# Kernel tuning notes

Hardware: AMD Instinct MI355X
Metric: run time of the kernel (lower is better)

## Reference

```python
import jax, jax.numpy as jnp
import numpy as np

H = 2048          # hidden_size
HK = 16           # linear_num_key_heads
HV = 32           # linear_num_value_heads
DK = 128          # linear_key_head_dim
DV = 128          # linear_value_head_dim
KW = 4            # linear_conv_kernel_dim
KEY_DIM = HK * DK   # 2048
VAL_DIM = HV * DV   # 4096
CONV_DIM = 2 * KEY_DIM + VAL_DIM  # 8192
T = 4096
EPS = 1e-6


def setup_inputs() -> dict:
    key = jax.random.key(0)
    ks = jax.random.split(key, 8)
    w = lambda k, shape, sc=0.02: (jax.random.normal(k, shape, jnp.float32) * sc)
    return {
        "hidden_states": jax.random.normal(ks[0], (T, H), jnp.float32),
        "W_qkvz": w(ks[1], (H, 2 * KEY_DIM + 2 * VAL_DIM)),   # q,k,v,z merged proj
        "W_ba": w(ks[2], (H, 2 * HV)),                        # b,a merged proj
        "conv_w": w(ks[3], (CONV_DIM, KW), 0.1),              # depthwise causal conv
        "A_log": jnp.log(jax.random.uniform(ks[4], (HV,), jnp.float32, 1.0, 16.0)),
        "dt_bias": jnp.ones((HV,), jnp.float32),
        "norm_w": jnp.ones((DV,), jnp.float32),
        "W_out": w(ks[5], (VAL_DIM, H)),
    }


def _l2norm(x):
    return x * jax.lax.rsqrt(jnp.sum(x * x, axis=-1, keepdims=True) + 1e-6)


def reference(hidden_states, W_qkvz, W_ba, conv_w, A_log, dt_bias, norm_w, W_out):
    T_ = hidden_states.shape[0]
    # 1. merged input projections
    qkvz = hidden_states @ W_qkvz                     # [T, 2*key+2*val]
    ba = hidden_states @ W_ba                         # [T, 2*HV]
    q, k, v, z = jnp.split(qkvz, [KEY_DIM, 2 * KEY_DIM, 2 * KEY_DIM + VAL_DIM], axis=-1)
    b, a = jnp.split(ba, 2, axis=-1)

    # 2. short causal depthwise conv1d over q|k|v (z is NOT convolved), then SiLU
    qkv = jnp.concatenate([q, k, v], axis=-1)         # [T, CONV_DIM]
    xp = jnp.pad(qkv, ((KW - 1, 0), (0, 0)))
    y = sum(xp[j:j + T_] * conv_w[:, j] for j in range(KW))
    qkv = jax.nn.silu(y)
    q, k, v = jnp.split(qkv, [KEY_DIM, 2 * KEY_DIM], axis=-1)

    q = _l2norm(q.reshape(T_, HK, DK)) * (DK ** -0.5)
    k = _l2norm(k.reshape(T_, HK, DK))
    v = v.reshape(T_, HV, DV)
    z = z.reshape(T_, HV, DV)

    # GQA-style head expansion
    r = HV // HK
    q = jnp.repeat(q, r, axis=1)                      # [T, HV, DK]
    k = jnp.repeat(k, r, axis=1)

    # gating / delta coefficients
    g = -jnp.exp(A_log) * jax.nn.softplus(a + dt_bias)  # [T, HV] log-decay
    beta = jax.nn.sigmoid(b)                            # [T, HV]

    # 3. gated delta rule recurrence: S_t = exp(g_t)*S + beta_t*k_t(v_t - k_t^T exp(g_t) S)
    def step(S, inp):
        q_t, k_t, v_t, g_t, b_t = inp
        S = S * jnp.exp(g_t)[:, None, None]             # [HV, DK, DV]
        kv = jnp.einsum('hd,hdv->hv', k_t, S)
        delta = (v_t - kv) * b_t[:, None]
        S = S + jnp.einsum('hd,hv->hdv', k_t, delta)
        o_t = jnp.einsum('hd,hdv->hv', q_t, S)
        return S, o_t

    S0 = jnp.zeros((HV, DK, DV), jnp.float32)
    _, o = jax.lax.scan(step, S0, (q, k, v, g, beta))   # o: [T, HV, DV]

    # 4. gated RMSNorm (norm_before_gate=True): rmsnorm(o)*w, then * silu(z)
    var = jnp.mean(o * o, axis=-1, keepdims=True)
    o = o * jax.lax.rsqrt(var + EPS) * norm_w
    o = o * jax.nn.silu(z)

    # 5. output projection
    return o.reshape(T_, VAL_DIM) @ W_out
```

## Files before the change

### kernel.cpp

```cpp
#include <hip/hip_runtime.h>
#include <hip/hip_bf16.h>

#define T_LEN 4096
#define H_DIM 2048
#define HKn 16
#define HVn 32
#define DKn 128
#define DVn 128
#define KEY_DIM 2048
#define VAL_DIM 4096

typedef unsigned int u32;
typedef unsigned short u16;
typedef __attribute__((ext_vector_type(8))) short bf16x8;
typedef __attribute__((ext_vector_type(4))) float f32x4;

__device__ __forceinline__ u16 f2bf(float x){
  u32 u = __float_as_uint(x);
  u32 r = (u + 0x7fffu + ((u>>16)&1u)) >> 16;
  return (u16)r;
}
__device__ __forceinline__ float bf2f(u32 b){ return __uint_as_float(b<<16); }
__device__ __forceinline__ u32 packbf(float a, float b){ return (u32)f2bf(a) | ((u32)f2bf(b)<<16); }

__global__ __launch_bounds__(256) void k_cvt(const float* __restrict__ in, u16* __restrict__ out, int n){
  int i = (blockIdx.x*256 + threadIdx.x)*8;
  if (i >= n) return;
  float4 a = *(const float4*)(in+i);
  float4 b = *(const float4*)(in+i+4);
  uint4 o;
  o.x = packbf(a.x,a.y); o.y = packbf(a.z,a.w);
  o.z = packbf(b.x,b.y); o.w = packbf(b.z,b.w);
  *(uint4*)(out+i) = o;
}

__global__ __launch_bounds__(256) void k_tcvt(const float* __restrict__ in, u16* __restrict__ out, int R, int C){
  __shared__ float tile[32][33];
  int c0 = blockIdx.x*32, r0 = blockIdx.y*32;
  int tx = threadIdx.x & 31, ty = threadIdx.x >> 5;
#pragma unroll
  for (int i=0;i<4;++i) tile[ty+8*i][tx] = in[(size_t)(r0+ty+8*i)*C + c0+tx];
  __syncthreads();
#pragma unroll
  for (int i=0;i<4;++i) out[(size_t)(c0+ty+8*i)*R + r0+tx] = f2bf(tile[tx][ty+8*i]);
}

__global__ __launch_bounds__(256) void k_ba(const float* __restrict__ X, const float* __restrict__ W,
    const float* __restrict__ A_log, const float* __restrict__ dt_bias,
    float* __restrict__ gT, float* __restrict__ bT){
  int tid = threadIdx.x;
  int t = blockIdx.x*4 + (tid>>6);
  int j = tid & 63;
  const float* xr = X + (size_t)t*H_DIM;
  float acc = 0.f;
  for (int k=0;k<H_DIM;k+=4){
    float4 xv = *(const float4*)(xr+k);
    acc += xv.x*W[(size_t)(k+0)*64 + j];
    acc += xv.y*W[(size_t)(k+1)*64 + j];
    acc += xv.z*W[(size_t)(k+2)*64 + j];
    acc += xv.w*W[(size_t)(k+3)*64 + j];
  }
  if (j < HVn) {
    bT[(size_t)j*T_LEN + t] = 1.f/(1.f+__expf(-acc));
  } else {
    int h = j - HVn;
    float x = acc + dt_bias[h];
    float sp = (x > 20.f) ? x : log1pf(__expf(x));
    gT[(size_t)h*T_LEN + t] = -__expf(A_log[h]) * sp;
  }
}

typedef const __attribute__((address_space(1))) u32* gas_t;
typedef __attribute__((address_space(3))) u32* las_t;
__device__ __forceinline__ void gld16(const void* g, void* l){
  __builtin_amdgcn_global_load_lds((gas_t)g, (las_t)l, 16, 0, 0);
}
__device__ __forceinline__ f32x4 mf(bf16x8 a, bf16x8 b, f32x4 c){
  return __builtin_amdgcn_mfma_f32_16x16x32_bf16(a,b,c,0,0,0);
}

#define G2_LDS 131072
#define SWX(a) ((a) ^ ((((a)>>9)&1)<<5))

template<int WRITE_BF16>
__global__ __launch_bounds__(512) void k_g256(const u16* __restrict__ A, const u16* __restrict__ BT,
    void* __restrict__ C1, void* __restrict__ C2, int NS, int M, int N, int K){
  extern __shared__ char sm[];
  const int tid=threadIdx.x, lane=tid&63, wave=tid>>6;
  const int fr=lane&15, fq=lane>>4;
  const int wm=wave>>2, wn=wave&3;
  const int nbm = M>>8, nwg = nbm*(N>>8);
  const int cpx = nwg>>3;
  const int swz = ((int)blockIdx.x & 7)*cpx + ((int)blockIdx.x >> 3);
  const int m0 = (swz % nbm) << 8, n0 = (swz / nbm) << 8;
  const int NK = K >> 5;

  f32x4 acc[8][4];
#pragma unroll
  for (int i=0;i<8;++i)
#pragma unroll
    for (int j=0;j<4;++j) acc[i][j] = (f32x4){0.f,0.f,0.f,0.f};

  auto stageA=[&](int kt){
    char* base = sm + (size_t)(kt&3)*32768;
#pragma unroll
    for (int ld=0; ld<2; ++ld){
      int p = ld*8192 + wave*1024 + lane*16;
      int a = SWX(p);
      gld16((const char*)A + ((size_t)(m0 + (a>>6))*K + kt*32)*2 + (a&63), base + p);
    }
  };
  auto stageB=[&](int kt){
    char* base = sm + (size_t)(kt&3)*32768 + 16384;
#pragma unroll
    for (int ld=0; ld<2; ++ld){
      int p = ld*8192 + wave*1024 + lane*16;
      int a = SWX(p);
      gld16((const char*)BT + ((size_t)(n0 + (a>>6))*K + kt*32)*2 + (a&63), base + p);
    }
  };

  stageA(0); stageB(0); stageA(1); stageB(1); stageA(2); stageB(2);
  __syncthreads();

  for (int kt=0; kt<NK; ++kt){
    const char* bufA = sm + (size_t)(kt&3)*32768;
    const char* bufB = bufA + 16384;
    bf16x8 bfr[4], afr[4];
#pragma unroll
    for (int j=0;j<4;++j){
      int a = (wn*64 + j*16 + fr)*64 + fq*16;
      bfr[j] = *(const bf16x8*)(bufB + SWX(a));
    }
#pragma unroll
    for (int i=0;i<4;++i){
      int a = (wm*128 + i*16 + fr)*64 + fq*16;
      afr[i] = *(const bf16x8*)(bufA + SWX(a));
    }
    if (kt+3 < NK) stageA(kt+3);
    asm volatile("s_barrier" ::: "memory");
    __builtin_amdgcn_s_setprio(1);
#pragma unroll
    for (int i=0;i<4;++i)
#pragma unroll
      for (int j=0;j<4;++j) acc[i][j] = mf(afr[i], bfr[j], acc[i][j]);
    __builtin_amdgcn_s_setprio(0);
    asm volatile("s_barrier" ::: "memory");
#pragma unroll
    for (int i=0;i<4;++i){
      int a = (wm*128 + 64 + i*16 + fr)*64 + fq*16;
      afr[i] = *(const bf16x8*)(bufA + SWX(a));
    }
    if (kt+3 < NK) stageB(kt+3);
    asm volatile("s_barrier" ::: "memory");
    __builtin_amdgcn_s_setprio(1);
#pragma unroll
    for (int i=0;i<4;++i)
#pragma unroll
      for (int j=0;j<4;++j) acc[4+i][j] = mf(afr[i], bfr[j], acc[4+i][j]);
    __builtin_amdgcn_s_setprio(0);
    asm volatile("s_waitcnt vmcnt(8)" ::: "memory");
    asm volatile("s_barrier" ::: "memory");
  }

#pragma unroll
  for (int mt=0; mt<8; ++mt)
#pragma unroll
    for (int nt=0; nt<4; ++nt){
      int row = m0 + wm*128 + mt*16 + fq*4;
      int col = n0 + wn*64 + nt*16 + fr;
#pragma unroll
      for (int r=0;r<4;++r){
        float v = acc[mt][nt][r];
        if (col < NS){
          if (WRITE_BF16) ((u16*)C1)[(size_t)(row+r)*NS + col] = f2bf(v);
          else            ((float*)C1)[(size_t)(row+r)*NS + col] = v;
        } else {
          if (WRITE_BF16) ((u16*)C2)[(size_t)(row+r)*(N-NS) + col-NS] = f2bf(v);
          else            ((float*)C2)[(size_t)(row+r)*(N-NS) + col-NS] = v;
        }
      }
    }
}

template<int WRITE_BF16>
__global__ __launch_bounds__(256) void k_gemm(const u16* __restrict__ A, const u16* __restrict__ BT,
                                              void* __restrict__ C1, void* __restrict__ C2, int NS,
                                              int M, int N, int K){
  __shared__ __align__(16) u16 As[128*32];
  __shared__ __align__(16) u16 Bs[128*32];
  int tid = threadIdx.x, lane = tid & 63, wave = tid >> 6;
  int wr = wave >> 1, wc = wave & 1;
  int m0 = blockIdx.x*128, n0 = blockIdx.y*128;
  int fr = lane & 15, fq = lane >> 4;
  f32x4 zero = {0.f,0.f,0.f,0.f};
  f32x4 acc[4][4];
#pragma unroll
  for (int m=0;m<4;++m)
#pragma unroll
    for (int n=0;n<4;++n) acc[m][n] = zero;

  for (int kt=0; kt<K; kt+=32){
#pragma unroll
    for (int it=0; it<2; ++it){
      int c = (it*4 + wave)*64 + lane;
      int row = c >> 2, kc = (c & 3) << 3;
      gld16(A  + (size_t)(m0+row)*K + kt + kc, (char*)As + (size_t)(it*4+wave)*1024);
      gld16(BT + (size_t)(n0+row)*K + kt + kc, (char*)Bs + (size_t)(it*4+wave)*1024);
    }
    __syncthreads();
    bf16x8 af[4], bff[4];
#pragma unroll
    for (int m=0;m<4;++m) af[m]  = *(const bf16x8*)(As + (wr*64 + m*16 + fr)*32 + fq*8);
#pragma unroll
    for (int n=0;n<4;++n) bff[n] = *(const bf16x8*)(Bs + (wc*64 + n*16 + fr)*32 + fq*8);
#pragma unroll
    for (int m=0;m<4;++m)
#pragma unroll
      for (int n=0;n<4;++n)
        acc[m][n] = mf(af[m], bff[n], acc[m][n]);
    __syncthreads();
  }
#pragma unroll
  for (int m=0;m<4;++m)
#pragma unroll
    for (int n=0;n<4;++n){
      int row = m0 + wr*64 + m*16 + fq*4;
      int col = n0 + wc*64 + n*16 + fr;
#pragma unroll
      for (int r=0;r<4;++r){
        float v = acc[m][n][r];
        if (col < NS){
          if (WRITE_BF16) ((u16*)C1)[(size_t)(row+r)*NS + col] = f2bf(v);
          else            ((float*)C1)[(size_t)(row+r)*NS + col] = v;
        } else {
          if (WRITE_BF16) ((u16*)C2)[(size_t)(row+r)*(N-NS) + col-NS] = f2bf(v);
          else            ((float*)C2)[(size_t)(row+r)*(N-NS) + col-NS] = v;
        }
      }
    }
}

__global__ __launch_bounds__(256) void k_conv(const u16* __restrict__ qkv, const float* __restrict__ cw,
    u16* __restrict__ qn, u16* __restrict__ kn, u16* __restrict__ vv){
  int t = blockIdx.x;
  int region = blockIdx.y;
  int c = region*2048 + threadIdx.x*8;
  float wgt[8][4];
#pragma unroll
  for (int i=0;i<8;++i){
    float4 wv = *(const float4*)(cw + (size_t)(c+i)*4);
    wgt[i][0]=wv.x; wgt[i][1]=wv.y; wgt[i][2]=wv.z; wgt[i][3]=wv.w;
  }
  float y[8];
#pragma unroll
  for (int i=0;i<8;++i) y[i]=0.f;
#pragma unroll
  for (int j=0;j<4;++j){
    int tt = t + j - 3;
    if (tt < 0) continue;
    uint4 raw = *(const uint4*)(qkv + (size_t)tt*8192 + c);
    float xv[8];
    xv[0]=bf2f(raw.x&0xffffu); xv[1]=bf2f(raw.x>>16);
    xv[2]=bf2f(raw.y&0xffffu); xv[3]=bf2f(raw.y>>16);
    xv[4]=bf2f(raw.z&0xffffu); xv[5]=bf2f(raw.z>>16);
    xv[6]=bf2f(raw.w&0xffffu); xv[7]=bf2f(raw.w>>16);
#pragma unroll
    for (int i=0;i<8;++i) y[i] += xv[i]*wgt[i][j];
  }
#pragma unroll
  for (int i=0;i<8;++i){ y[i] = y[i] / (1.f + __expf(-y[i])); }

  if (region <= 1){
    float ss = 0.f;
#pragma unroll
    for (int i=0;i<8;++i) ss += y[i]*y[i];
    ss += __shfl_xor(ss,1); ss += __shfl_xor(ss,2);
    ss += __shfl_xor(ss,4); ss += __shfl_xor(ss,8);
    float sc = 1.f/sqrtf(ss + 1e-6f);
    if (region==0) sc *= 0.08838834764831845f;
#pragma unroll
    for (int i=0;i<8;++i) y[i]*=sc;
    u16* dst = (region==0 ? qn : kn) + (size_t)t*KEY_DIM + (c - region*2048);
    *(uint4*)dst = make_uint4(packbf(y[0],y[1]),packbf(y[2],y[3]),packbf(y[4],y[5]),packbf(y[6],y[7]));
  } else {
    u16* dst = vv + (size_t)t*VAL_DIM + (c - 4096);
    *(uint4*)dst = make_uint4(packbf(y[0],y[1]),packbf(y[2],y[3]),packbf(y[4],y[5]),packbf(y[6],y[7]));
  }
}

#define P1_K    0
#define P1_Q    16384
#define P1_KT   32768
#define P1_NBP  49152
#define P1_AQ   57344
#define P1_DT   65536
#define P1_WMT  73728
#define P1_NBD  81920
#define P1_TII  86016
#define P1_R1T  90112
#define P1_TAB  94208
#define P1_SIZE 95296

#define SW7(r,cb) ((cb) ^ (((r)&7)<<4))
#define SW3(r,cb) ((cb) ^ (((r)&3)<<4))
#define aK(r,cb)   (P1_K   + (r)*256 + SW7(r,cb))
#define aQ2(r,cb)  (P1_Q   + (r)*256 + SW7(r,cb))
#define aKT(d,cb)  (P1_KT  + (d)*128 + SW7(d,cb))
#define aNBP(t,cb) (P1_NBP + (t)*128 + SW7(t,cb))
#define aAQ(t,cb)  (P1_AQ  + (t)*128 + SW7(t,cb))
#define aDT(s,cb)  (P1_DT  + (s)*128 + SW7(s,cb))
#define aWMT(s,cb) (P1_WMT + (s)*128 + SW7(s,cb))
#define aTII(b,r,cb) (P1_TII + (b)*1024 + (r)*64 + SW3(r,cb))
#define aR1T(v,cb)   (P1_R1T + (v)*64 + SW3(v,cb))

__global__ __launch_bounds__(256) void k_prep(const u16* __restrict__ qn, const u16* __restrict__ kn,
    const float* __restrict__ gT, const float* __restrict__ bT,
    u16* __restrict__ aqmg, u16* __restrict__ kwmg, float* __restrict__ tabg){
  extern __shared__ char sm[];
  const int tid=threadIdx.x, lane=tid&63, wave=tid>>6;
  const int fr=lane&15, fq=lane>>4;
  const int b=blockIdx.x, h=b>>6, c=b&63, kh=h>>1;
  const f32x4 z4={0.f,0.f,0.f,0.f};
  for (int off=P1_DT+tid*16; off<P1_TAB; off+=4096) *(uint4*)(sm+off)=make_uint4(0,0,0,0);
  {
    int srow = wave*4 + (lane>>4);
    int pb = (lane&15)*16;
#pragma unroll
    for (int r=0;r<4;++r){
      int row=r*16+srow;
      int gcb = pb ^ ((row&7)<<4);
      gld16((const char*)kn + ((size_t)((c<<6)+row)*KEY_DIM + kh*DKn)*2 + gcb, sm + P1_K + r*4096 + wave*1024);
      gld16((const char*)qn + ((size_t)((c<<6)+row)*KEY_DIM + kh*DKn)*2 + gcb, sm + P1_Q + r*4096 + wave*1024);
    }
  }
  float* TB=(float*)(sm+P1_TAB);
  if (wave==0){
    int t=lane;
    float gv=gT[(size_t)h*T_LEN+(c<<6)+t];
    float bv=bT[(size_t)h*T_LEN+(c<<6)+t];
    float s=gv;
    for(int o2=1;o2<64;o2<<=1){ float u=__shfl_up(s,o2,64); if(lane>=o2) s+=u; }
    float cgL=__shfl(s,63,64);
    float gam=__expf(s);
    TB[t]=s; TB[64+t]=gam; TB[128+t]=__expf(cgL-s); TB[192+t]=bv;
    float* tg=tabg+(size_t)b*192;
    tg[t]=gam; tg[64+t]=bv;
    if(t==0) tg[128]=__expf(cgL);
  }
  __syncthreads();
#pragma unroll
  for (int dd=0;dd<2;++dd){
    int tp=tid&31, d0=((tid>>5)+dd*8)*8;
    bf16x8 r0=*(const bf16x8*)(sm+aK(2*tp,d0*2));
    bf16x8 r1=*(const bf16x8*)(sm+aK(2*tp+1,d0*2));
#pragma unroll
    for(int j=0;j<8;++j){
      u32 pk=((u32)(u16)r0[j])|((u32)(u16)r1[j]<<16);
      *(u32*)(sm+aKT(d0+j,tp*4))=pk;
    }
  }
  const int ra=(wave>>1)*32, rb=(wave&1)*32;
  f32x4 kq[2][2], qk[2][2];
#pragma unroll
  for(int ta=0;ta<2;++ta)
#pragma unroll
  for(int tb=0;tb<2;++tb){ kq[ta][tb]=z4; qk[ta][tb]=z4; }
#pragma unroll
  for(int kk=0;kk<4;++kk){
    int cb=kk*64+fq*16;
    bf16x8 Ak0=*(const bf16x8*)(sm+aK(ra+fr,cb));
    bf16x8 Ak1=*(const bf16x8*)(sm+aK(ra+16+fr,cb));
    bf16x8 Aq0=*(const bf16x8*)(sm+aQ2(ra+fr,cb));
    bf16x8 Aq1=*(const bf16x8*)(sm+aQ2(ra+16+fr,cb));
    bf16x8 Bk0=*(const bf16x8*)(sm+aK(rb+fr,cb));
    bf16x8 Bk1=*(const bf16x8*)(sm+aK(rb+16+fr,cb));
    if(ra>=rb)      { kq[0][0]=mf(Ak0,Bk0,kq[0][0]); qk[0][0]=mf(Aq0,Bk0,qk[0][0]); }
    if(ra>=rb+16)   { kq[0][1]=mf(Ak0,Bk1,kq[0][1]); qk[0][1]=mf(Aq0,Bk1,qk[0][1]); }
    if(ra+16>=rb)   { kq[1][0]=mf(Ak1,Bk0,kq[1][0]); qk[1][0]=mf(Aq1,Bk0,qk[1][0]); }
    if(ra+16>=rb+16){ kq[1][1]=mf(Ak1,Bk1,kq[1][1]); qk[1][1]=mf(Aq1,Bk1,qk[1][1]); }
  }
  {
    const float* cg=TB; const float* Be=TB+192;
#pragma unroll
    for(int ta=0;ta<2;++ta)
#pragma unroll
    for(int tb=0;tb<2;++tb){
      int tab=ra+16*ta, tbb=rb+16*tb;
#pragma unroll
      for(int p=0;p<4;++p){
        int t=tab+fq*4+p, s2=tbb+fr;
        float e=__expf(cg[t]-cg[s2]);
        float nv=(s2<t)? -Be[t]*kq[ta][tb][p]*e : 0.f;
        *(u16*)(sm+aNBP(t,s2*2)) = (tbb<tab)? f2bf(nv):(u16)0;
        if(tbb==tab) ((float*)(sm+P1_NBD))[(tab>>4)*256+(fq*4+p)*16+fr]=nv;
        float av=(s2<=t)? qk[ta][tb][p]*e : 0.f;
        *(u16*)(sm+aAQ(t,s2*2)) = f2bf(av);
      }
    }
  }
  __syncthreads();
  {
    int r=lane&15;
    const float* nb=(const float*)(sm+P1_NBD)+wave*256+r*16;
    float n[16], t_[16];
#pragma unroll
    for(int j=0;j<16;++j){ n[j]=nb[j]; t_[j]=(j==r)?1.f:0.f; }
#pragma unroll
    for(int s=0;s<15;++s){
      float tsj[16];
#pragma unroll
      for(int j=0;j<16;++j)
        tsj[j]=__int_as_float(__builtin_amdgcn_ds_bpermute(s*4,__float_as_int(t_[j])));
      if(r>s){
#pragma unroll
        for(int j=0;j<16;++j) t_[j]=fmaf(n[s],tsj[j],t_[j]);
      }
    }
    if(lane<16){
      u32 pk[8];
#pragma unroll
      for(int j=0;j<8;++j) pk[j]=packbf(t_[2*j],t_[2*j+1]);
      *(uint4*)(sm+aTII(wave,r,0)) =make_uint4(pk[0],pk[1],pk[2],pk[3]);
      *(uint4*)(sm+aTII(wave,r,16))=make_uint4(pk[4],pk[5],pk[6],pk[7]);
    }
  }
  __syncthreads();
  {
    const float* WV=TB+128;
    int vb=16*wave;
    for(int i=0;i<4;++i){
      f32x4 acc;
#pragma unroll
      for(int p=0;p<4;++p) acc[p]=(vb+fr==16*i+fq*4+p)?1.f:0.f;
      int np=(i+1)>>1;
      for(int jp=0;jp<np;++jp){
        bf16x8 A=*(const bf16x8*)(sm+aNBP(16*i+fr,jp*64+fq*16));
        bf16x8 B=*(const bf16x8*)(sm+aDT(vb+fr,jp*64+fq*16));
        acc=mf(A,B,acc);
      }
      uint2 w1; w1.x=packbf(acc[0],acc[1]); w1.y=packbf(acc[2],acc[3]);
      *(uint2*)(sm+aR1T(vb+fr,fq*8))=w1;
      bf16x8 At=*(const bf16x8*)(sm+aTII(i,fr,fq*16));
      bf16x8 Bt=*(const bf16x8*)(sm+aR1T(vb+fr,fq*16));
      f32x4 dl=mf(At,Bt,z4);
      int s0=16*i+fq*4;
      uint2 wd; wd.x=packbf(dl[0],dl[1]); wd.y=packbf(dl[2],dl[3]);
      *(uint2*)(sm+aDT(vb+fr,s0*2))=wd;
      uint2 ww; ww.x=packbf(dl[0]*WV[s0],dl[1]*WV[s0+1]); ww.y=packbf(dl[2]*WV[s0+2],dl[3]*WV[s0+3]);
      *(uint2*)(sm+aWMT(vb+fr,s0*2))=ww;
    }
  }
  __syncthreads();
  {
    u16* aout = aqmg + (size_t)b*4096;
#pragma unroll
    for(int ts=0;ts<4;++ts){
      f32x4 acc=z4;
#pragma unroll
      for(int jp=0;jp<2;++jp){
        bf16x8 A=*(const bf16x8*)(sm+aAQ(16*wave+fr,jp*64+fq*16));
        bf16x8 B=*(const bf16x8*)(sm+aDT(16*ts+fr,jp*64+fq*16));
        acc=mf(A,B,acc);
      }
#pragma unroll
      for(int p=0;p<4;++p){
        int t=16*wave+fq*4+p, s=16*ts+fr;
        aout[(t*128 + ((s*2)^((t&7)<<4)))>>1]=f2bf(acc[p]);
      }
    }
    u16* kout = kwmg + (size_t)b*8192;
#pragma unroll
    for(int j=0;j<2;++j){
      int dt=wave+4*j;
#pragma unroll
      for(int st=0;st<4;++st){
        f32x4 acc=z4;
#pragma unroll
        for(int jp=0;jp<2;++jp){
          bf16x8 A=*(const bf16x8*)(sm+aKT(16*dt+fr,jp*64+fq*16));
          bf16x8 B=*(const bf16x8*)(sm+aWMT(16*st+fr,jp*64+fq*16));
          acc=mf(A,B,acc);
        }
#pragma unroll
        for(int p=0;p<4;++p){
          int d=16*dt+fq*4+p, s=16*st+fr;
          kout[(d*128 + ((s*2)^((d&7)<<4)))>>1]=f2bf(acc[p]);
        }
      }
    }
  }
}

#define P2_K(b)   ((b)*16384)
#define P2_Q(b)   (32768 + (b)*16384)
#define P2_W(b)   (65536 + (b)*16384)
#define P2_M(b)   (98304 + (b)*8192)
#define P2_TAB(b) (114688 + (b)*1024)
#define P2_ST(b)  (116736 + (b)*4096)
#define P2_R0T    124928
#define P2_SIZE   126976

#define bKx(b,r,cb)  (P2_K(b) + (r)*256 + SW7(r,cb))
#define bQx(b,r,cb)  (P2_Q(b) + (r)*256 + SW7(r,cb))
#define bWx(b,d,cb)  (P2_W(b) + (d)*128 + SW7(d,cb))
#define bMx(b,t,cb)  (P2_M(b) + (t)*128 + SW7(t,cb))
#define bSTx(b,v,cb) (P2_ST(b) + (v)*256 + SW7(v,cb))
#define bRx(v,cb)    (P2_R0T + (v)*128 + SW7(v,cb))

__global__ __launch_bounds__(256) void k_state(const u16* __restrict__ qn, const u16* __restrict__ kn,
    const u16* __restrict__ vv, const u16* __restrict__ aqmg, const u16* __restrict__ kwmg,
    const float* __restrict__ tabg, float* __restrict__ o){
  extern __shared__ char sm[];
  const int tid=threadIdx.x, lane=tid&63, wave=tid>>6;
  const int fr=lane&15, fq=lane>>4;
  const int h=blockIdx.x&31, vs=(blockIdx.x>>5)*16, kh=h>>1;
  const f32x4 z4={0.f,0.f,0.f,0.f};
  for(int off=116736+tid*16; off<124928; off+=4096) *(uint4*)(sm+off)=make_uint4(0,0,0,0);

  auto stage=[&](int c,int b){
    int srow=wave*4+(lane>>4);
    int pb2=(lane&15)*16;
#pragma unroll
    for(int r=0;r<4;++r){
      int row=r*16+srow;
      int gcb=pb2^((row&7)<<4);
      gld16((const char*)kn + ((size_t)((c<<6)+row)*KEY_DIM + kh*DKn)*2 + gcb, sm + P2_K(b)+r*4096+wave*1024);
      gld16((const char*)qn + ((size_t)((c<<6)+row)*KEY_DIM + kh*DKn)*2 + gcb, sm + P2_Q(b)+r*4096+wave*1024);
    }
    const char* wsrc=(const char*)kwmg + (size_t)(h*64+c)*16384;
#pragma unroll
    for(int r=0;r<4;++r)
      gld16(wsrc + r*4096 + wave*1024 + lane*16, sm + P2_W(b)+r*4096+wave*1024);
    const char* msrc=(const char*)aqmg + (size_t)(h*64+c)*8192;
#pragma unroll
    for(int r=0;r<2;++r)
      gld16(msrc + r*4096 + wave*1024 + lane*16, sm + P2_M(b)+r*4096+wave*1024);
    if(wave==0)
      gld16((const char*)tabg + (size_t)(h*64+c)*768 + lane*16, sm + P2_TAB(b));
  };
  u16 vl[4];
  auto loadV=[&](int c){
#pragma unroll
    for(int p=0;p<4;++p)
      vl[p]=vv[(size_t)((c<<6)+16*wave+fq*4+p)*VAL_DIM + h*DVn + vs + fr];
  };

  f32x4 S0=z4, S1=z4;
  stage(0,0); loadV(0);
  __syncthreads();

  for(int c=0;c<64;++c){
    int b=c&1;
    const float* TBf=(const float*)(sm+P2_TAB(b));
    f32x4 ks=z4;
#pragma unroll
    for(int kk=0;kk<4;++kk)
      ks=mf(*(const bf16x8*)(sm+bKx(b,16*wave+fr,kk*64+fq*16)),
            *(const bf16x8*)(sm+bSTx(b,fr,kk*64+fq*16)), ks);
    float r0v[4];
#pragma unroll
    for(int p=0;p<4;++p){
      int t=16*wave+fq*4+p;
      r0v[p]=TBf[64+t]*(bf2f(vl[p]) - TBf[t]*ks[p]);
    }
    uint2 rw; rw.x=packbf(r0v[0],r0v[1]); rw.y=packbf(r0v[2],r0v[3]);
    *(uint2*)(sm+bRx(fr,32*wave+8*fq))=rw;
    __syncthreads();
    if(c<63) stage(c+1,b^1);
    f32x4 qs=z4;
#pragma unroll
    for(int kk=0;kk<4;++kk)
      qs=mf(*(const bf16x8*)(sm+bQx(b,16*wave+fr,kk*64+fq*16)),
            *(const bf16x8*)(sm+bSTx(b,fr,kk*64+fq*16)), qs);
#pragma unroll
    for(int p=0;p<4;++p) qs[p]*=TBf[16*wave+fq*4+p];
#pragma unroll
    for(int jp=0;jp<2;++jp)
      qs=mf(*(const bf16x8*)(sm+bMx(b,16*wave+fr,jp*64+fq*16)),
            *(const bf16x8*)(sm+bRx(fr,jp*64+fq*16)), qs);
#pragma unroll
    for(int p=0;p<4;++p)
      o[(size_t)((c<<6)+16*wave+fq*4+p)*VAL_DIM + h*DVn + vs + fr]=qs[p];
    if(c<63) loadV(c+1);
    float gl=TBf[128];
    S0[0]*=gl;S0[1]*=gl;S0[2]*=gl;S0[3]*=gl;
    S1[0]*=gl;S1[1]*=gl;S1[2]*=gl;S1[3]*=gl;
#pragma unroll
    for(int jp=0;jp<2;++jp){
      bf16x8 Br=*(const bf16x8*)(sm+bRx(fr,jp*64+fq*16));
      S0=mf(*(const bf16x8*)(sm+bWx(b,16*wave+fr,jp*64+fq*16)), Br, S0);
      S1=mf(*(const bf16x8*)(sm+bWx(b,16*(wave+4)+fr,jp*64+fq*16)), Br, S1);
    }
    uint2 s0w; s0w.x=packbf(S0[0],S0[1]); s0w.y=packbf(S0[2],S0[3]);
    *(uint2*)(sm+bSTx(b^1,fr,32*wave+8*fq))=s0w;
    uint2 s1w; s1w.x=packbf(S1[0],S1[1]); s1w.y=packbf(S1[2],S1[3]);
    *(uint2*)(sm+bSTx(b^1,fr,32*(wave+4)+8*fq))=s1w;
    __syncthreads();
  }
}

__global__ __launch_bounds__(256) void k_gnorm(const float* __restrict__ o, const u16* __restrict__ zq,
    const float* __restrict__ nw, u16* __restrict__ og){
  int t = blockIdx.x;
  int base = threadIdx.x*16;
  const float* src = o + (size_t)t*VAL_DIM + base;
  float x[16];
#pragma unroll
  for (int i=0;i<4;++i){
    float4 f = *(const float4*)(src + i*4);
    x[i*4+0]=f.x; x[i*4+1]=f.y; x[i*4+2]=f.z; x[i*4+3]=f.w;
  }
  float ss=0.f;
#pragma unroll
  for (int i=0;i<16;++i) ss += x[i]*x[i];
  ss += __shfl_xor(ss,1); ss += __shfl_xor(ss,2); ss += __shfl_xor(ss,4);
  float rs = 1.f/sqrtf(ss*(1.f/128.f) + 1e-6f);
  const u16* zp = zq + (size_t)t*VAL_DIM + base;
  uint4 z0 = *(const uint4*)zp;
  uint4 z1 = *(const uint4*)(zp+8);
  u32 zr[8] = {z0.x,z0.y,z0.z,z0.w,z1.x,z1.y,z1.z,z1.w};
  u32 outw[8];
#pragma unroll
  for (int p=0;p<8;++p){
    float za = bf2f(zr[p]&0xffffu), zb = bf2f(zr[p]>>16);
    float sa = za/(1.f+__expf(-za)), sb = zb/(1.f+__expf(-zb));
    int i0 = p*2, i1 = p*2+1;
    float oa = x[i0]*rs*nw[(base+i0)&127]*sa;
    float ob = x[i1]*rs*nw[(base+i1)&127]*sb;
    outw[p] = packbf(oa, ob);
  }
  uint4* dst = (uint4*)(og + (size_t)t*VAL_DIM + base);
  dst[0] = make_uint4(outw[0],outw[1],outw[2],outw[3]);
  dst[1] = make_uint4(outw[4],outw[5],outw[6],outw[7]);
}

extern "C" void kernel_launch(void* const* d_in, const int* in_sizes, int n_in,
                              void* d_out, int out_size, void* d_ws, size_t ws_size,
                              hipStream_t stream) {
  const float* hidden  = (const float*)d_in[0];
  const float* W_qkvz  = (const float*)d_in[1];
  const float* W_ba    = (const float*)d_in[2];
  const float* conv_w  = (const float*)d_in[3];
  const float* A_log   = (const float*)d_in[4];
  const float* dt_bias = (const float*)d_in[5];
  const float* norm_w  = (const float*)d_in[6];
  const float* W_out   = (const float*)d_in[7];

  char* w = (char*)d_ws;
  size_t need = 252706816;
  if (ws_size < need) return;

  u16*   Xb   = (u16*)(w + 0);
  u16*   W1T  = (u16*)(w + 16777216);
  u16*   QKV  = (u16*)(w + 67108864);
  u16*   Z    = (u16*)(w + 134217728);
  u16*   QN   = (u16*)(w + 167772160);
  u16*   KN   = (u16*)(w + 184549376);
  u16*   V    = (u16*)(w + 201326592);
  u16*   WoT  = (u16*)(w + 234881024);
  float* GTb  = (float*)(w + 251658240);
  float* BTb  = (float*)(w + 252182528);
  float* O    = (float*)(w + 0);
  u16*   AQMg = (u16*)(w + 67108864);
  u16*   KWMg = (u16*)(w + 83886080);
  float* TABg = (float*)(w + 117440512);
  u16*   OG   = (u16*)(w + 167772160);

  static int smem_set = 0;
  if (!smem_set){
    hipFuncSetAttribute((const void*)k_prep,  hipFuncAttributeMaxDynamicSharedMemorySize, P1_SIZE);
    hipFuncSetAttribute((const void*)k_state, hipFuncAttributeMaxDynamicSharedMemorySize, P2_SIZE);
    hipFuncSetAttribute((const void*)k_g256<1>, hipFuncAttributeMaxDynamicSharedMemorySize, G2_LDS);
    smem_set = 1;
  }

  k_cvt<<<4096,256,0,stream>>>(hidden, Xb, T_LEN*H_DIM);
  k_tcvt<<<dim3(12288/32, H_DIM/32),256,0,stream>>>(W_qkvz, W1T, H_DIM, 12288);
  k_tcvt<<<dim3(H_DIM/32, VAL_DIM/32),256,0,stream>>>(W_out, WoT, VAL_DIM, H_DIM);
  k_ba<<<T_LEN/4,256,0,stream>>>(hidden, W_ba, A_log, dt_bias, GTb, BTb);
  k_g256<1><<<768,512,G2_LDS,stream>>>(Xb, W1T, QKV, Z, 8192, T_LEN, 12288, H_DIM);
  k_conv<<<dim3(T_LEN,4),256,0,stream>>>(QKV, conv_w, QN, KN, V);
  k_prep<<<2048,256,P1_SIZE,stream>>>(QN, KN, GTb, BTb, AQMg, KWMg, TABg);
  k_state<<<256,256,P2_SIZE,stream>>>(QN, KN, V, AQMg, KWMg, TABg, O);
  k_gnorm<<<T_LEN,256,0,stream>>>(O, Z, norm_w, OG);
  k_gemm<0><<<dim3(T_LEN/128, H_DIM/128),256,0,stream>>>(OG, WoT, d_out, d_out, H_DIM, T_LEN, H_DIM, VAL_DIM);
}
```

Baseline: 820.4 us.

## Software-pipeline LDS fragment loads in k_g256 and use it for output projection

Restructures the k_g256 main loop so the B fragments and the first A half for the next k-tile are read from LDS during the current tile, double-buffering register fragments, and moves the vmcnt wait earlier. It also drops the simple 128x128 k_gemm and runs the output projection through the 256-tile k_g256<0> with 128 blocks. The aim is to hide LDS latency behind MFMA work and use the faster tiled GEMM for the second projection. The cost is more register pressure, and only 128 blocks for the output GEMM, which may underfill the GPU's compute units.

Result: no change. 818.0 us (-0.3%).

```diff
diff --git a/kernel.cpp b/kernel.cpp
--- a/kernel.cpp
+++ b/kernel.cpp
@@ -123,44 +123,64 @@
   stageA(0); stageB(0); stageA(1); stageB(1); stageA(2); stageB(2);
   __syncthreads();
 
+  bf16x8 bcur[4], bnxt[4], a0f[4], a1f[4];
+  {
+    const char* bufA = sm;
+    const char* bufB = sm + 16384;
+#pragma unroll
+    for (int j=0;j<4;++j){
+      int a = (wn*64 + j*16 + fr)*64 + fq*16;
+      bcur[j] = *(const bf16x8*)(bufB + SWX(a));
+    }
+#pragma unroll
+    for (int i=0;i<4;++i){
+      int a = (wm*128 + i*16 + fr)*64 + fq*16;
+      a0f[i] = *(const bf16x8*)(bufA + SWX(a));
+    }
+  }
+
   for (int kt=0; kt<NK; ++kt){
     const char* bufA = sm + (size_t)(kt&3)*32768;
-    const char* bufB = bufA + 16384;
-    bf16x8 bfr[4], afr[4];
-#pragma unroll
-    for (int j=0;j<4;++j){
-      int a = (wn*64 + j*16 + fr)*64 + fq*16;
-      bfr[j] = *(const bf16x8*)(bufB + SWX(a));
-    }
+    if (kt+3 < NK) stageA(kt+3);
 #pragma unroll
     for (int i=0;i<4;++i){
-      int a = (wm*128 + i*16 + fr)*64 + fq*16;
-      afr[i] = *(const bf16x8*)(bufA + SWX(a));
-    }
-    if (kt+3 < NK) stageA(kt+3);
+      int a = (wm*128 + 64 + i*16 + fr)*64 + fq*16;
+      a1f[i] = *(const bf16x8*)(bufA + SWX(a));
+    }
+    asm volatile("s_waitcnt vmcnt(6)" ::: "memory");
     asm volatile("s_barrier" ::: "memory");
     __builtin_amdgcn_s_setprio(1);
 #pragma unroll
     for (int i=0;i<4;++i)
 #pragma unroll
-      for (int j=0;j<4;++j) acc[i][j] = mf(afr[i], bfr[j], acc[i][j]);
+      for (int j=0;j<4;++j) acc[i][j] = mf(a0f[i], bcur[j], acc[i][j]);
     __builtin_amdgcn_s_setprio(0);
     asm volatile("s_barrier" ::: "memory");
-#pragma unroll
-    for (int i=0;i<4;++i){
-      int a = (wm*128 + 64 + i*16 + fr)*64 + fq*16;
-      afr[i] = *(const bf16x8*)(bufA + SWX(a));
-    }
     if (kt+3 < NK) stageB(kt+3);
+    if (kt+1 < NK){
+      const char* nA = sm + (size_t)((kt+1)&3)*32768;
+      const char* nB = nA + 16384;
+#pragma unroll
+      for (int j=0;j<4;++j){
+        int a = (wn*64 + j*16 + fr)*64 + fq*16;
+        bnxt[j] = *(const bf16x8*)(nB + SWX(a));
+      }
+#pragma unroll
+      for (int i=0;i<4;++i){
+        int a = (wm*128 + i*16 + fr)*64 + fq*16;
+        a0f[i] = *(const bf16x8*)(nA + SWX(a));
+      }
+    }
     asm volatile("s_barrier" ::: "memory");
     __builtin_amdgcn_s_setprio(1);
 #pragma unroll
     for (int i=0;i<4;++i)
 #pragma unroll
-      for (int j=0;j<4;++j) acc[4+i][j] = mf(afr[i], bfr[j], acc[4+i][j]);
+      for (int j=0;j<4;++j) acc[4+i][j] = mf(a1f[i], bcur[j], acc[4+i][j]);
     __builtin_amdgcn_s_setprio(0);
-    asm volatile("s_waitcnt vmcnt(8)" ::: "memory");
     asm volatile("s_barrier" ::: "memory");
+#pragma unroll
+    for (int j=0;j<4;++j) bcur[j] = bnxt[j];
   }
 
 #pragma unroll
@@ -172,64 +192,6 @@
 #pragma unroll
       for (int r=0;r<4;++r){
         float v = acc[mt][nt][r];
-        if (col < NS){
-          if (WRITE_BF16) ((u16*)C1)[(size_t)(row+r)*NS + col] = f2bf(v);
-          else            ((float*)C1)[(size_t)(row+r)*NS + col] = v;
-        } else {
-          if (WRITE_BF16) ((u16*)C2)[(size_t)(row+r)*(N-NS) + col-NS] = f2bf(v);
-          else            ((float*)C2)[(size_t)(row+r)*(N-NS) + col-NS] = v;
-        }
-      }
-    }
-}
-
-template<int WRITE_BF16>
-__global__ __launch_bounds__(256) void k_gemm(const u16* __restrict__ A, const u16* __restrict__ BT,
-                                              void* __restrict__ C1, void* __restrict__ C2, int NS,
-                                              int M, int N, int K){
-  __shared__ __align__(16) u16 As[128*32];
-  __shared__ __align__(16) u16 Bs[128*32];
-  int tid = threadIdx.x, lane = tid & 63, wave = tid >> 6;
-  int wr = wave >> 1, wc = wave & 1;
-  int m0 = blockIdx.x*128, n0 = blockIdx.y*128;
-  int fr = lane & 15, fq = lane >> 4;
-  f32x4 zero = {0.f,0.f,0.f,0.f};
-  f32x4 acc[4][4];
-#pragma unroll
-  for (int m=0;m<4;++m)
-#pragma unroll
-    for (int n=0;n<4;++n) acc[m][n] = zero;
-
-  for (int kt=0; kt<K; kt+=32){
-#pragma unroll
-    for (int it=0; it<2; ++it){
-      int c = (it*4 + wave)*64 + lane;
-      int row = c >> 2, kc = (c & 3) << 3;
-      gld16(A  + (size_t)(m0+row)*K + kt + kc, (char*)As + (size_t)(it*4+wave)*1024);
-      gld16(BT + (size_t)(n0+row)*K + kt + kc, (char*)Bs + (size_t)(it*4+wave)*1024);
-    }
-    __syncthreads();
-    bf16x8 af[4], bff[4];
-#pragma unroll
-    for (int m=0;m<4;++m) af[m]  = *(const bf16x8*)(As + (wr*64 + m*16 + fr)*32 + fq*8);
-#pragma unroll
-    for (int n=0;n<4;++n) bff[n] = *(const bf16x8*)(Bs + (wc*64 + n*16 + fr)*32 + fq*8);
-#pragma unroll
-    for (int m=0;m<4;++m)
-#pragma unroll
-      for (int n=0;n<4;++n)
-        acc[m][n] = mf(af[m], bff[n], acc[m][n]);
-    __syncthreads();
-  }
-#pragma unroll
-  for (int m=0;m<4;++m)
-#pragma unroll
-    for (int n=0;n<4;++n){
-      int row = m0 + wr*64 + m*16 + fq*4;
-      int col = n0 + wc*64 + n*16 + fr;
-#pragma unroll
-      for (int r=0;r<4;++r){
-        float v = acc[m][n][r];
         if (col < NS){
           if (WRITE_BF16) ((u16*)C1)[(size_t)(row+r)*NS + col] = f2bf(v);
           else            ((float*)C1)[(size_t)(row+r)*NS + col] = v;
@@ -672,6 +634,7 @@
     hipFuncSetAttribute((const void*)k_prep,  hipFuncAttributeMaxDynamicSharedMemorySize, P1_SIZE);
     hipFuncSetAttribute((const void*)k_state, hipFuncAttributeMaxDynamicSharedMemorySize, P2_SIZE);
     hipFuncSetAttribute((const void*)k_g256<1>, hipFuncAttributeMaxDynamicSharedMemorySize, G2_LDS);
+    hipFuncSetAttribute((const void*)k_g256<0>, hipFuncAttributeMaxDynamicSharedMemorySize, G2_LDS);
     smem_set = 1;
   }
 
@@ -684,5 +647,5 @@
   k_prep<<<2048,256,P1_SIZE,stream>>>(QN, KN, GTb, BTb, AQMg, KWMg, TABg);
   k_state<<<256,256,P2_SIZE,stream>>>(QN, KN, V, AQMg, KWMg, TABg, O);
   k_gnorm<<<T_LEN,256,0,stream>>>(O, Z, norm_w, OG);
-  k_gemm<0><<<dim3(T_LEN/128, H_DIM/128),256,0,stream>>>(OG, WoT, d_out, d_out, H_DIM, T_LEN, H_DIM, VAL_DIM);
-}
+  k_g256<0><<<128,512,G2_LDS,stream>>>(OG, WoT, d_out, d_out, H_DIM, T_LEN, H_DIM, VAL_DIM);
+}
```
